# Kernel optimization log

Hardware: AMD Instinct MI355X
Metric: run time of the kernel (lower is better)

Reference implementation:

```python
import jax, jax.numpy as jnp
import numpy as np

T = 2048
C = 2048
N_HEAD = 16
HEAD_DIM = C // N_HEAD


def setup_inputs() -> dict:
    key = jax.random.key(0)
    k1, k2, k3 = jax.random.split(key, 3)
    x = jax.random.normal(k1, (T, C), dtype=jnp.float32)
    # eqx.nn.Linear weight convention: (out_features, in_features)
    W_attn = jax.random.normal(k2, (3 * C, C), dtype=jnp.float32) * (1.0 / np.sqrt(C))
    W_proj = jax.random.normal(k3, (C, C), dtype=jnp.float32) * (1.0 / np.sqrt(C))
    return {"x": x, "W_attn": W_attn, "W_proj": W_proj}


def reference(x, W_attn, W_proj):
    # qkv projection: (T, 3C)
    qkv = x @ W_attn.T
    q, k, v = jnp.split(qkv, 3, axis=-1)
    # reshape to (H, T, d)
    q = q.reshape(T, N_HEAD, HEAD_DIM).transpose(1, 0, 2)
    k = k.reshape(T, N_HEAD, HEAD_DIM).transpose(1, 0, 2)
    v = v.reshape(T, N_HEAD, HEAD_DIM).transpose(1, 0, 2)
    # scaled causal attention: (H, T, T)
    att = jnp.einsum('htd,hsd->hts', q, k)
    causal_mask = jnp.triu(jnp.ones((T, T), dtype=bool), k=1)  # mask future keys
    att = jnp.where(causal_mask, -jnp.inf, att)
    att = jax.nn.softmax(att / jnp.sqrt(jnp.float32(HEAD_DIM)), axis=-1)
    # attention output: (H, T, d) -> (T, C)
    out = jnp.einsum('hts,hsd->htd', att, v)
    out = out.transpose(1, 0, 2).reshape(T, C)
    return out @ W_proj.T
```

## Files before the change

### kernel.cpp

```cpp
#include <hip/hip_runtime.h>
#include <cstdint>

using bx8 = __attribute__((ext_vector_type(8))) __bf16;
using us8 = __attribute__((ext_vector_type(8))) unsigned short;
using fl8 = __attribute__((ext_vector_type(8))) float;
using fx4 = __attribute__((ext_vector_type(4))) float;

static __device__ inline unsigned short f2bf(float f) {
  unsigned u = __builtin_bit_cast(unsigned, f);
  unsigned r = 0x7FFFu + ((u >> 16) & 1u);
  return (unsigned short)((u + r) >> 16);
}
static __device__ inline float bf2f(unsigned short s) {
  return __builtin_bit_cast(float, (unsigned)s << 16);
}

static __device__ inline fx4 mfma16(bx8 a, bx8 b, fx4 c) {
  return __builtin_amdgcn_mfma_f32_16x16x32_bf16(a, b, c, 0, 0, 0);
}

static __device__ inline void gload16(const void* g, void* lds) {
  __builtin_amdgcn_global_load_lds(
      (const __attribute__((address_space(1))) void*)g,
      (__attribute__((address_space(3))) void*)lds,
      16, 0, 0);
}
#define VMCNT(n) asm volatile("s_waitcnt vmcnt(" #n ")" ::: "memory")
static __device__ inline void wave_barrier() {
  __builtin_amdgcn_sched_barrier(0);
  __builtin_amdgcn_s_barrier();
  __builtin_amdgcn_sched_barrier(0);
}

#define DPP_ROR(x, k) __builtin_bit_cast(float, __builtin_amdgcn_update_dpp( \
    __builtin_bit_cast(int, x), __builtin_bit_cast(int, x), 0x120 | (k), 0xF, 0xF, false))

static __device__ inline float rowmax16(float v) {
  v = fmaxf(v, DPP_ROR(v, 1));
  v = fmaxf(v, DPP_ROR(v, 2));
  v = fmaxf(v, DPP_ROR(v, 4));
  v = fmaxf(v, DPP_ROR(v, 8));
  return v;
}
static __device__ inline float rowsum16(float v) {
  v += DPP_ROR(v, 1);
  v += DPP_ROR(v, 2);
  v += DPP_ROR(v, 4);
  v += DPP_ROR(v, 8);
  return v;
}

__global__ __launch_bounds__(256) void f2b_kernel(const float* __restrict__ in,
                                                  unsigned short* __restrict__ out,
                                                  int n) {
  int i = (blockIdx.x * 256 + threadIdx.x) * 4;
  if (i >= n) return;
  float4 v = *reinterpret_cast<const float4*>(in + i);
  ushort4 o;
  o.x = f2bf(v.x); o.y = f2bf(v.y); o.z = f2bf(v.z); o.w = f2bf(v.w);
  *reinterpret_cast<ushort4*>(out + i) = o;
}

__global__ __launch_bounds__(512, 2) void gemm256(const unsigned short* __restrict__ A,
                                                  const unsigned short* __restrict__ B,
                                                  unsigned short* __restrict__ C,
                                                  int M, int N, int K) {
  __shared__ unsigned short lds[4][2][256 * 32];

  const int tid = threadIdx.x;
  const int w = tid >> 6, l = tid & 63;
  const int l16 = l & 15, lg = l >> 4;
  const int wr = w >> 2, wc = w & 3;
  const long mb = (long)blockIdx.y * 256, nb = (long)blockIdx.x * 256;

  const int lr = l >> 2;
  const int sw = (((l & 3) ^ (lr & 3)) * 8);
  const unsigned short* Ag = A + (mb + w * 32 + lr) * (long)K + sw;
  const unsigned short* Bg = B + (nb + w * 32 + lr) * (long)K + sw;

  const int rdcol = ((lg ^ (l16 & 3)) * 16);

  const fx4 fz = {0.f, 0.f, 0.f, 0.f};
  fx4 acc[8][4];
#pragma unroll
  for (int i = 0; i < 8; ++i)
#pragma unroll
    for (int j = 0; j < 4; ++j) acc[i][j] = fz;

  const int nt = K >> 5;

  auto stage = [&](int tp) {
    const int db = tp & 3;
    const unsigned short* as = Ag + tp * 32;
    const unsigned short* bs = Bg + tp * 32;
    char* al = (char*)&lds[db][0][0] + w * 32 * 64;
    char* bl = (char*)&lds[db][1][0] + w * 32 * 64;
    gload16(as, al);
    gload16(as + 16 * (long)K, al + 1024);
    gload16(bs, bl);
    gload16(bs + 16 * (long)K, bl + 1024);
  };

  auto compute = [&](int bt) {
    const char* Ab = (const char*)&lds[bt][0][0] + (wr * 128 + l16) * 64 + rdcol;
    const char* Bb = (const char*)&lds[bt][1][0] + (wc * 64 + l16) * 64 + rdcol;
    bx8 bf[4];
#pragma unroll
    for (int nf = 0; nf < 4; ++nf)
      bf[nf] = *reinterpret_cast<const bx8*>(Bb + nf * 1024);
    __builtin_amdgcn_s_setprio(1);
#pragma unroll
    for (int mf = 0; mf < 8; ++mf) {
      bx8 av = *reinterpret_cast<const bx8*>(Ab + mf * 1024);
#pragma unroll
      for (int nf = 0; nf < 4; ++nf)
        acc[mf][nf] = mfma16(av, bf[nf], acc[mf][nf]);
    }
    __builtin_amdgcn_s_setprio(0);
  };

  stage(0); stage(1); stage(2);
  VMCNT(8);
  wave_barrier();

  int t = 0;
  for (; t < nt - 3; ++t) {
    stage(t + 3);
    compute(t & 3);
    VMCNT(8);
    wave_barrier();
  }
  compute(t & 3); VMCNT(4); wave_barrier(); ++t;
  compute(t & 3); VMCNT(0); wave_barrier(); ++t;
  compute(t & 3);

#pragma unroll
  for (int mf = 0; mf < 8; ++mf)
#pragma unroll
    for (int nf = 0; nf < 4; ++nf)
#pragma unroll
      for (int r = 0; r < 4; ++r) {
        const long row = mb + wr * 128 + mf * 16 + lg * 4 + r;
        const long col = nb + wc * 64 + nf * 16 + l16;
        C[row * N + col] = f2bf(acc[mf][nf][r]);
      }
}

template <typename T> struct RegOf { using type = us8; };
template <> struct RegOf<float>  { using type = fl8; };

template <typename T>
static __device__ inline typename RegOf<T>::type load8(const T* p) {
  return *reinterpret_cast<const typename RegOf<T>::type*>(p);
}
static __device__ inline us8 toBf(us8 v) { return v; }
static __device__ inline us8 toBf(fl8 f) {
  us8 o;
#pragma unroll
  for (int j = 0; j < 8; ++j) {
    __bf16 b = (__bf16)f[j];
    o[j] = __builtin_bit_cast(unsigned short, b);
  }
  return o;
}

template <typename TA, typename TB, bool F32OUT>
__global__ __launch_bounds__(256) void gemm_bt(const TA* __restrict__ A,
                                               const TB* __restrict__ B,
                                               void* __restrict__ Cp,
                                               int M, int N, int K) {
  __shared__ alignas(16) unsigned short As[128 * 64];
  __shared__ alignas(16) unsigned short Bs[128 * 64];
  const int tid = threadIdx.x;
  const int w = tid >> 6, l = tid & 63;
  const int l16 = l & 15, lg = l >> 4;
  const int wr = w >> 1, wc = w & 1;
  const long mb = (long)blockIdx.y * 128, nb = (long)blockIdx.x * 128;

  const fx4 fz = {0.f, 0.f, 0.f, 0.f};
  fx4 acc[4][4];
#pragma unroll
  for (int i = 0; i < 4; ++i)
#pragma unroll
    for (int j = 0; j < 4; ++j) acc[i][j] = fz;

  const int sr  = tid >> 3;
  const int sc8 = (tid & 7) * 8;
  const int wbc = sc8 * 2;

  typename RegOf<TA>::type rA[4];
  typename RegOf<TB>::type rB[4];

#pragma unroll
  for (int p = 0; p < 4; ++p) {
    const int row = p * 32 + sr;
    rA[p] = load8(A + (mb + row) * (long)K + sc8);
    rB[p] = load8(B + (nb + row) * (long)K + sc8);
  }

  for (int k0 = 0; k0 < K; k0 += 64) {
    __syncthreads();
#pragma unroll
    for (int p = 0; p < 4; ++p) {
      const int row = p * 32 + sr;
      const int eo = row * 64 + ((wbc ^ ((row & 7) << 4)) >> 1);
      *reinterpret_cast<us8*>(&As[eo]) = toBf(rA[p]);
      *reinterpret_cast<us8*>(&Bs[eo]) = toBf(rB[p]);
    }
    if (k0 + 64 < K) {
#pragma unroll
      for (int p = 0; p < 4; ++p) {
        const int row = p * 32 + sr;
        rA[p] = load8(A + (mb + row) * (long)K + k0 + 64 + sc8);
        rB[p] = load8(B + (nb + row) * (long)K + k0 + 64 + sc8);
      }
    }
    __syncthreads();
#pragma unroll
    for (int kk = 0; kk < 2; ++kk) {
      bx8 a[4], b[4];
#pragma unroll
      for (int mf = 0; mf < 4; ++mf) {
        const int ra = wr * 64 + mf * 16 + l16;
        const int bc = kk * 64 + lg * 16;
        a[mf] = *reinterpret_cast<const bx8*>(&As[ra * 64 + ((bc ^ ((ra & 7) << 4)) >> 1)]);
      }
#pragma unroll
      for (int nf = 0; nf < 4; ++nf) {
        const int rb_ = wc * 64 + nf * 16 + l16;
        const int bc = kk * 64 + lg * 16;
        b[nf] = *reinterpret_cast<const bx8*>(&Bs[rb_ * 64 + ((bc ^ ((rb_ & 7) << 4)) >> 1)]);
      }
#pragma unroll
      for (int mf = 0; mf < 4; ++mf)
#pragma unroll
        for (int nf = 0; nf < 4; ++nf)
          acc[mf][nf] = mfma16(a[mf], b[nf], acc[mf][nf]);
    }
  }

#pragma unroll
  for (int mf = 0; mf < 4; ++mf)
#pragma unroll
    for (int nf = 0; nf < 4; ++nf)
#pragma unroll
      for (int r = 0; r < 4; ++r) {
        const long row = mb + wr * 64 + mf * 16 + lg * 4 + r;
        const long col = nb + wc * 64 + nf * 16 + l16;
        if (F32OUT)
          ((float*)Cp)[row * N + col] = acc[mf][nf][r];
        else
          ((unsigned short*)Cp)[row * N + col] = f2bf(acc[mf][nf][r]);
      }
}

__global__ __launch_bounds__(256) void fa_kernel(const unsigned short* __restrict__ qkv,
                                                 unsigned short* __restrict__ out,
                                                 unsigned short* __restrict__ Obuf,
                                                 float* __restrict__ ML) {
  __shared__ alignas(16) unsigned short Ks[64 * 136];
  __shared__ alignas(16) unsigned short Vt[128 * 72];
  __shared__ alignas(16) unsigned short Ps[4][16 * 72];

  const int id = blockIdx.x;
  int h, qt, t0, t1;
  bool partial;
  if (id < 512) {
    const int p = id >> 1, c = id & 1;
    qt = 31 - (p >> 4); h = p & 15;
    const int nt0 = (qt + 2) >> 1;
    t0 = c ? nt0 : 0;
    t1 = c ? (qt + 1) : nt0;
    partial = true;
  } else {
    const int s = id - 512;
    qt = 15 - (s >> 4); h = s & 15;
    t0 = 0; t1 = qt + 1;
    partial = false;
  }
  const int qb = qt * 64;

  const int tid = threadIdx.x;
  const int w = tid >> 6, l = tid & 63;
  const int l16 = l & 15, lg = l >> 4;
  const fx4 fz = {0.f, 0.f, 0.f, 0.f};

  const int kr = tid >> 4, kc8 = (tid & 15) * 8;
  const int kv = tid & 63, d0v = (tid >> 6) * 32;

  bx8 qf[4];
  {
    const long qrow = qb + w * 16 + l16;
    const unsigned short* qp = qkv + qrow * 6144L + h * 128 + lg * 8;
#pragma unroll
    for (int kc = 0; kc < 4; ++kc)
      qf[kc] = *reinterpret_cast<const bx8*>(qp + kc * 32);
  }

  fx4 o_acc[8];
#pragma unroll
  for (int i = 0; i < 8; ++i) o_acc[i] = fz;
  float m_r[4] = {-3e38f, -3e38f, -3e38f, -3e38f};
  float l_r[4] = {0.f, 0.f, 0.f, 0.f};

  us8 rK[4], rV[4];
  {
    const long kvb = (long)t0 * 64;
#pragma unroll
    for (int p = 0; p < 4; ++p)
      rK[p] = *reinterpret_cast<const us8*>(qkv + (kvb + p * 16 + kr) * 6144L + 2048 + h * 128 + kc8);
#pragma unroll
    for (int i = 0; i < 4; ++i)
      rV[i] = *reinterpret_cast<const us8*>(qkv + (kvb + kv) * 6144L + 4096 + h * 128 + d0v + i * 8);
  }

  for (int t = t0; t < t1; ++t) {
    __syncthreads();

#pragma unroll
    for (int p = 0; p < 4; ++p)
      *reinterpret_cast<us8*>(&Ks[(p * 16 + kr) * 136 + kc8]) = rK[p];
#pragma unroll
    for (int i = 0; i < 4; ++i)
#pragma unroll
      for (int j = 0; j < 8; ++j)
        Vt[(d0v + i * 8 + j) * 72 + kv] = rV[i][j];

    if (t + 1 < t1) {
      const long kvb = (long)(t + 1) * 64;
#pragma unroll
      for (int p = 0; p < 4; ++p)
        rK[p] = *reinterpret_cast<const us8*>(qkv + (kvb + p * 16 + kr) * 6144L + 2048 + h * 128 + kc8);
#pragma unroll
      for (int i = 0; i < 4; ++i)
        rV[i] = *reinterpret_cast<const us8*>(qkv + (kvb + kv) * 6144L + 4096 + h * 128 + d0v + i * 8);
    }
    __syncthreads();

    fx4 s[4];
#pragma unroll
    for (int nf = 0; nf < 4; ++nf) s[nf] = fz;
#pragma unroll
    for (int kc = 0; kc < 4; ++kc) {
#pragma unroll
      for (int nf = 0; nf < 4; ++nf) {
        const int rl = nf * 16 + l16;
        bx8 kb = *reinterpret_cast<const bx8*>(&Ks[rl * 136 + kc * 32 + lg * 8]);
        s[nf] = mfma16(qf[kc], kb, s[nf]);
      }
    }

    if (t == qt) {
#pragma unroll
      for (int nf = 0; nf < 4; ++nf) {
        const int kv_abs = t * 64 + nf * 16 + l16;
#pragma unroll
        for (int r = 0; r < 4; ++r) {
          const int q_abs = qb + w * 16 + lg * 4 + r;
          if (kv_abs > q_abs) s[nf][r] = -3e38f;
        }
      }
    }

    const float sc2 = 0.1275173831f;
    float pv[4][4];
#pragma unroll
    for (int r = 0; r < 4; ++r) {
      float rm = fmaxf(fmaxf(s[0][r], s[1][r]), fmaxf(s[2][r], s[3][r]));
      rm = rowmax16(rm);
      const float mn = fmaxf(m_r[r], rm);
      const float fac = exp2f((m_r[r] - mn) * sc2);
      m_r[r] = mn;
      float rs = 0.f;
#pragma unroll
      for (int nf = 0; nf < 4; ++nf) {
        const float p = exp2f((s[nf][r] - mn) * sc2);
        pv[nf][r] = p;
        rs += p;
      }
      rs = rowsum16(rs);
      l_r[r] = l_r[r] * fac + rs;
#pragma unroll
      for (int nf = 0; nf < 8; ++nf) o_acc[nf][r] *= fac;
    }

    unsigned short* psw = &Ps[w][0];
#pragma unroll
    for (int nf = 0; nf < 4; ++nf)
#pragma unroll
      for (int r = 0; r < 4; ++r)
        psw[(lg * 4 + r) * 72 + nf * 16 + l16] = f2bf(pv[nf][r]);

    bx8 pa[2];
#pragma unroll
    for (int kc = 0; kc < 2; ++kc)
      pa[kc] = *reinterpret_cast<const bx8*>(&psw[l16 * 72 + kc * 32 + lg * 8]);

#pragma unroll
    for (int nf = 0; nf < 8; ++nf) {
#pragma unroll
      for (int kc = 0; kc < 2; ++kc) {
        bx8 vb = *reinterpret_cast<const bx8*>(&Vt[(nf * 16 + l16) * 72 + kc * 32 + lg * 8]);
        o_acc[nf] = mfma16(pa[kc], vb, o_acc[nf]);
      }
    }
  }

  if (!partial) {
#pragma unroll
    for (int nf = 0; nf < 8; ++nf)
#pragma unroll
      for (int r = 0; r < 4; ++r) {
        const long row = qb + w * 16 + lg * 4 + r;
        const long col = h * 128 + nf * 16 + l16;
        out[row * 2048 + col] = f2bf(o_acc[nf][r] / l_r[r]);
      }
  } else {
    unsigned short* ob = Obuf + (long)id * 8192;
#pragma unroll
    for (int nf = 0; nf < 8; ++nf)
#pragma unroll
      for (int r = 0; r < 4; ++r) {
        const int row = w * 16 + lg * 4 + r;
        ob[row * 128 + nf * 16 + l16] = f2bf(o_acc[nf][r]);
      }
    if (l16 == 0) {
#pragma unroll
      for (int r = 0; r < 4; ++r) {
        const int row = w * 16 + lg * 4 + r;
        ML[((long)id * 64 + row) * 2 + 0] = m_r[r];
        ML[((long)id * 64 + row) * 2 + 1] = l_r[r];
      }
    }
  }
}

__global__ __launch_bounds__(256) void fa_combine(const unsigned short* __restrict__ Obuf,
                                                  const float* __restrict__ ML,
                                                  unsigned short* __restrict__ out) {
  const int p = blockIdx.x;
  const int qt = 31 - (p >> 4), h = p & 15;
  const int tid = threadIdx.x;
  const int row = tid >> 2;
  const int c0 = (tid & 3) * 32;

  const long idA = 2 * p, idB = 2 * p + 1;
  const float mA = ML[(idA * 64 + row) * 2 + 0];
  const float lA = ML[(idA * 64 + row) * 2 + 1];
  const float mB = ML[(idB * 64 + row) * 2 + 0];
  const float lB = ML[(idB * 64 + row) * 2 + 1];
  const float sc2 = 0.1275173831f;
  const float m = fmaxf(mA, mB);
  const float fA = exp2f((mA - m) * sc2);
  const float fB = exp2f((mB - m) * sc2);
  const float inv = 1.0f / (lA * fA + lB * fB);
  const float cA = fA * inv, cB = fB * inv;

  const unsigned short* oa = Obuf + idA * 8192 + row * 128 + c0;
  const unsigned short* obp = Obuf + idB * 8192 + row * 128 + c0;
  unsigned short* dst = out + (long)(qt * 64 + row) * 2048 + h * 128 + c0;
#pragma unroll
  for (int j = 0; j < 4; ++j) {
    us8 a = *reinterpret_cast<const us8*>(oa + j * 8);
    us8 b = *reinterpret_cast<const us8*>(obp + j * 8);
    ushort4 o0, o1;
    float v0, v1, v2, v3;
    v0 = bf2f(a[0]) * cA + bf2f(b[0]) * cB;
    v1 = bf2f(a[1]) * cA + bf2f(b[1]) * cB;
    v2 = bf2f(a[2]) * cA + bf2f(b[2]) * cB;
    v3 = bf2f(a[3]) * cA + bf2f(b[3]) * cB;
    o0 = {f2bf(v0), f2bf(v1), f2bf(v2), f2bf(v3)};
    v0 = bf2f(a[4]) * cA + bf2f(b[4]) * cB;
    v1 = bf2f(a[5]) * cA + bf2f(b[5]) * cB;
    v2 = bf2f(a[6]) * cA + bf2f(b[6]) * cB;
    v3 = bf2f(a[7]) * cA + bf2f(b[7]) * cB;
    o1 = {f2bf(v0), f2bf(v1), f2bf(v2), f2bf(v3)};
    *reinterpret_cast<ushort4*>(dst + j * 8) = o0;
    *reinterpret_cast<ushort4*>(dst + j * 8 + 4) = o1;
  }
}

extern "C" void kernel_launch(void* const* d_in, const int* in_sizes, int n_in,
                              void* d_out, int out_size, void* d_ws, size_t ws_size,
                              hipStream_t stream) {
  const float* x  = (const float*)d_in[0];
  const float* Wa = (const float*)d_in[1];
  const float* Wp = (const float*)d_in[2];
  float* out = (float*)d_out;
  char* ws = (char*)d_ws;

  unsigned short* wab   = (unsigned short*)(ws);
  unsigned short* qkvb  = (unsigned short*)(ws + (24ull << 20));
  unsigned short* xb    = (unsigned short*)(ws + (48ull << 20));
  unsigned short* Obuf  = (unsigned short*)(ws);
  float*          ML    = (float*)(ws + (8ull << 20));
  unsigned short* attnb = (unsigned short*)(ws + (48ull << 20));

  f2b_kernel<<<4096, 256, 0, stream>>>(x, xb, 2048 * 2048);
  f2b_kernel<<<12288, 256, 0, stream>>>(Wa, wab, 6144 * 2048);

  gemm256<<<dim3(24, 8), 512, 0, stream>>>(xb, wab, qkvb, 2048, 6144, 2048);

  fa_kernel<<<768, 256, 0, stream>>>(qkvb, attnb, Obuf, ML);

  fa_combine<<<256, 256, 0, stream>>>(Obuf, ML, attnb);

  gemm_bt<unsigned short, float, true><<<dim3(16, 16), 256, 0, stream>>>(attnb, Wp, (void*)out, 2048, 2048, 2048);
}
```

Before: 180.0 us.

## Split attention KV range into fixed 8-tile chunks with generalized combine

Every query tile's KV range is now split into chunks of at most 8 tiles, giving 1280 flash-attention blocks that all write partial outputs, with a combine kernel that merges up to four partials per tile. This balances the causal workload across more blocks. The change also adds a lazy rescale that skips the running-max update and accumulator rescaling when the new row max stays within a threshold. It also reorganises the V transpose into vectorised 4-element LDS stores and uses the native bf16 convert for P. The cost is extra partial-output traffic and a combine pass over all tiles, including ones with a single chunk.

Result: no change. 182.9 us (+1.6%).

```diff
diff --git a/kernel.cpp b/kernel.cpp
--- a/kernel.cpp
+++ b/kernel.cpp
@@ -3,6 +3,7 @@
 
 using bx8 = __attribute__((ext_vector_type(8))) __bf16;
 using us8 = __attribute__((ext_vector_type(8))) unsigned short;
+using us4 = __attribute__((ext_vector_type(4))) unsigned short;
 using fl8 = __attribute__((ext_vector_type(8))) float;
 using fx4 = __attribute__((ext_vector_type(4))) float;
 
@@ -255,7 +256,6 @@
 }
 
 __global__ __launch_bounds__(256) void fa_kernel(const unsigned short* __restrict__ qkv,
-                                                 unsigned short* __restrict__ out,
                                                  unsigned short* __restrict__ Obuf,
                                                  float* __restrict__ ML) {
   __shared__ alignas(16) unsigned short Ks[64 * 136];
@@ -263,21 +263,14 @@
   __shared__ alignas(16) unsigned short Ps[4][16 * 72];
 
   const int id = blockIdx.x;
-  int h, qt, t0, t1;
-  bool partial;
-  if (id < 512) {
-    const int p = id >> 1, c = id & 1;
-    qt = 31 - (p >> 4); h = p & 15;
-    const int nt0 = (qt + 2) >> 1;
-    t0 = c ? nt0 : 0;
-    t1 = c ? (qt + 1) : nt0;
-    partial = true;
-  } else {
-    const int s = id - 512;
-    qt = 15 - (s >> 4); h = s & 15;
-    t0 = 0; t1 = qt + 1;
-    partial = false;
-  }
+  const int h = id & 15, i = id >> 4;
+  int qt, ck;
+  if (i < 32)      { qt = 31 - (i >> 2); ck = i & 3; }
+  else if (i < 56) { const int j = i - 32; qt = 23 - j / 3; ck = j % 3; }
+  else if (i < 72) { const int j = i - 56; qt = 15 - (j >> 1); ck = j & 1; }
+  else             { qt = 7 - (i - 72); ck = 0; }
+  const int t0 = ck * 8;
+  const int t1 = min(t0 + 8, qt + 1);
   const int qb = qt * 64;
 
   const int tid = threadIdx.x;
@@ -286,7 +279,7 @@
   const fx4 fz = {0.f, 0.f, 0.f, 0.f};
 
   const int kr = tid >> 4, kc8 = (tid & 15) * 8;
-  const int kv = tid & 63, d0v = (tid >> 6) * 32;
+  const int kg = tid & 15, db = tid >> 4;
 
   bx8 qf[4];
   {
@@ -299,7 +292,7 @@
 
   fx4 o_acc[8];
 #pragma unroll
-  for (int i = 0; i < 8; ++i) o_acc[i] = fz;
+  for (int i2 = 0; i2 < 8; ++i2) o_acc[i2] = fz;
   float m_r[4] = {-3e38f, -3e38f, -3e38f, -3e38f};
   float l_r[4] = {0.f, 0.f, 0.f, 0.f};
 
@@ -310,9 +303,11 @@
     for (int p = 0; p < 4; ++p)
       rK[p] = *reinterpret_cast<const us8*>(qkv + (kvb + p * 16 + kr) * 6144L + 2048 + h * 128 + kc8);
 #pragma unroll
-    for (int i = 0; i < 4; ++i)
-      rV[i] = *reinterpret_cast<const us8*>(qkv + (kvb + kv) * 6144L + 4096 + h * 128 + d0v + i * 8);
-  }
+    for (int p = 0; p < 4; ++p)
+      rV[p] = *reinterpret_cast<const us8*>(qkv + (kvb + kg * 4 + p) * 6144L + 4096 + h * 128 + db * 8);
+  }
+
+  const float sc2 = 0.1275173831f;
 
   for (int t = t0; t < t1; ++t) {
     __syncthreads();
@@ -321,10 +316,10 @@
     for (int p = 0; p < 4; ++p)
       *reinterpret_cast<us8*>(&Ks[(p * 16 + kr) * 136 + kc8]) = rK[p];
 #pragma unroll
-    for (int i = 0; i < 4; ++i)
-#pragma unroll
-      for (int j = 0; j < 8; ++j)
-        Vt[(d0v + i * 8 + j) * 72 + kv] = rV[i][j];
+    for (int j = 0; j < 8; ++j) {
+      us4 vw = {rV[0][j], rV[1][j], rV[2][j], rV[3][j]};
+      *reinterpret_cast<us4*>(&Vt[(db * 8 + j) * 72 + kg * 4]) = vw;
+    }
 
     if (t + 1 < t1) {
       const long kvb = (long)(t + 1) * 64;
@@ -332,8 +327,8 @@
       for (int p = 0; p < 4; ++p)
         rK[p] = *reinterpret_cast<const us8*>(qkv + (kvb + p * 16 + kr) * 6144L + 2048 + h * 128 + kc8);
 #pragma unroll
-      for (int i = 0; i < 4; ++i)
-        rV[i] = *reinterpret_cast<const us8*>(qkv + (kvb + kv) * 6144L + 4096 + h * 128 + d0v + i * 8);
+      for (int p = 0; p < 4; ++p)
+        rV[p] = *reinterpret_cast<const us8*>(qkv + (kvb + kg * 4 + p) * 6144L + 4096 + h * 128 + db * 8);
     }
     __syncthreads();
 
@@ -362,26 +357,44 @@
       }
     }
 
-    const float sc2 = 0.1275173831f;
-    float pv[4][4];
+    float rm_[4];
+    bool st = true;
 #pragma unroll
     for (int r = 0; r < 4; ++r) {
       float rm = fmaxf(fmaxf(s[0][r], s[1][r]), fmaxf(s[2][r], s[3][r]));
-      rm = rowmax16(rm);
-      const float mn = fmaxf(m_r[r], rm);
-      const float fac = exp2f((m_r[r] - mn) * sc2);
-      m_r[r] = mn;
-      float rs = 0.f;
-#pragma unroll
-      for (int nf = 0; nf < 4; ++nf) {
-        const float p = exp2f((s[nf][r] - mn) * sc2);
-        pv[nf][r] = p;
-        rs += p;
-      }
-      rs = rowsum16(rs);
-      l_r[r] = l_r[r] * fac + rs;
-#pragma unroll
-      for (int nf = 0; nf < 8; ++nf) o_acc[nf][r] *= fac;
+      rm_[r] = rowmax16(rm);
+      st = st && (rm_[r] - m_r[r] <= 62.7f);
+    }
+    float pv[4][4];
+    if (__all(st ? 1 : 0)) {
+#pragma unroll
+      for (int r = 0; r < 4; ++r) {
+        float rs = 0.f;
+#pragma unroll
+        for (int nf = 0; nf < 4; ++nf) {
+          const float p = exp2f((s[nf][r] - m_r[r]) * sc2);
+          pv[nf][r] = p;
+          rs += p;
+        }
+        l_r[r] += rowsum16(rs);
+      }
+    } else {
+#pragma unroll
+      for (int r = 0; r < 4; ++r) {
+        const float mn = fmaxf(m_r[r], rm_[r]);
+        const float fac = exp2f((m_r[r] - mn) * sc2);
+        m_r[r] = mn;
+        float rs = 0.f;
+#pragma unroll
+        for (int nf = 0; nf < 4; ++nf) {
+          const float p = exp2f((s[nf][r] - mn) * sc2);
+          pv[nf][r] = p;
+          rs += p;
+        }
+        l_r[r] = l_r[r] * fac + rowsum16(rs);
+#pragma unroll
+        for (int nf = 0; nf < 8; ++nf) o_acc[nf][r] *= fac;
+      }
     }
 
     unsigned short* psw = &Ps[w][0];
@@ -389,7 +402,8 @@
     for (int nf = 0; nf < 4; ++nf)
 #pragma unroll
       for (int r = 0; r < 4; ++r)
-        psw[(lg * 4 + r) * 72 + nf * 16 + l16] = f2bf(pv[nf][r]);
+        psw[(lg * 4 + r) * 72 + nf * 16 + l16] =
+            __builtin_bit_cast(unsigned short, (__bf16)pv[nf][r]);
 
     bx8 pa[2];
 #pragma unroll
@@ -406,31 +420,20 @@
     }
   }
 
-  if (!partial) {
-#pragma unroll
-    for (int nf = 0; nf < 8; ++nf)
-#pragma unroll
-      for (int r = 0; r < 4; ++r) {
-        const long row = qb + w * 16 + lg * 4 + r;
-        const long col = h * 128 + nf * 16 + l16;
-        out[row * 2048 + col] = f2bf(o_acc[nf][r] / l_r[r]);
-      }
-  } else {
-    unsigned short* ob = Obuf + (long)id * 8192;
-#pragma unroll
-    for (int nf = 0; nf < 8; ++nf)
-#pragma unroll
-      for (int r = 0; r < 4; ++r) {
-        const int row = w * 16 + lg * 4 + r;
-        ob[row * 128 + nf * 16 + l16] = f2bf(o_acc[nf][r]);
-      }
-    if (l16 == 0) {
-#pragma unroll
-      for (int r = 0; r < 4; ++r) {
-        const int row = w * 16 + lg * 4 + r;
-        ML[((long)id * 64 + row) * 2 + 0] = m_r[r];
-        ML[((long)id * 64 + row) * 2 + 1] = l_r[r];
-      }
+  unsigned short* ob = Obuf + (long)id * 8192;
+#pragma unroll
+  for (int nf = 0; nf < 8; ++nf)
+#pragma unroll
+    for (int r = 0; r < 4; ++r) {
+      const int row = w * 16 + lg * 4 + r;
+      ob[row * 128 + nf * 16 + l16] = f2bf(o_acc[nf][r]);
+    }
+  if (l16 == 0) {
+#pragma unroll
+    for (int r = 0; r < 4; ++r) {
+      const int row = w * 16 + lg * 4 + r;
+      ML[((long)id * 64 + row) * 2 + 0] = m_r[r];
+      ML[((long)id * 64 + row) * 2 + 1] = l_r[r];
     }
   }
 }
@@ -439,44 +442,72 @@
                                                   const float* __restrict__ ML,
                                                   unsigned short* __restrict__ out) {
   const int p = blockIdx.x;
-  const int qt = 31 - (p >> 4), h = p & 15;
+  const int qt = p >> 4, h = p & 15;
+  const int nc = (qt + 8) >> 3;
   const int tid = threadIdx.x;
   const int row = tid >> 2;
   const int c0 = (tid & 3) * 32;
-
-  const long idA = 2 * p, idB = 2 * p + 1;
-  const float mA = ML[(idA * 64 + row) * 2 + 0];
-  const float lA = ML[(idA * 64 + row) * 2 + 1];
-  const float mB = ML[(idB * 64 + row) * 2 + 0];
-  const float lB = ML[(idB * 64 + row) * 2 + 1];
   const float sc2 = 0.1275173831f;
-  const float m = fmaxf(mA, mB);
-  const float fA = exp2f((mA - m) * sc2);
-  const float fB = exp2f((mB - m) * sc2);
-  const float inv = 1.0f / (lA * fA + lB * fB);
-  const float cA = fA * inv, cB = fB * inv;
-
-  const unsigned short* oa = Obuf + idA * 8192 + row * 128 + c0;
-  const unsigned short* obp = Obuf + idB * 8192 + row * 128 + c0;
+
+  int ids[4];
+#pragma unroll
+  for (int k = 0; k < 4; ++k) {
+    int ib;
+    if (qt >= 24)      ib = (31 - qt) * 4 + k;
+    else if (qt >= 16) ib = 32 + (23 - qt) * 3 + k;
+    else if (qt >= 8)  ib = 56 + (15 - qt) * 2 + k;
+    else               ib = 72 + (7 - qt);
+    ids[k] = ib * 16 + h;
+  }
+
+  float mk[4], lk[4];
+  float m = -3e38f;
+#pragma unroll
+  for (int k = 0; k < 4; ++k)
+    if (k < nc) {
+      mk[k] = ML[((long)ids[k] * 64 + row) * 2 + 0];
+      lk[k] = ML[((long)ids[k] * 64 + row) * 2 + 1];
+      m = fmaxf(m, mk[k]);
+    }
+  float fk[4], denom = 0.f;
+#pragma unroll
+  for (int k = 0; k < 4; ++k)
+    if (k < nc) {
+      fk[k] = exp2f((mk[k] - m) * sc2);
+      denom += lk[k] * fk[k];
+    }
+  const float inv = 1.0f / denom;
+
+  float acc[32];
+#pragma unroll
+  for (int j = 0; j < 32; ++j) acc[j] = 0.f;
+#pragma unroll
+  for (int k = 0; k < 4; ++k)
+    if (k < nc) {
+      const unsigned short* ob = Obuf + (long)ids[k] * 8192 + row * 128 + c0;
+      const float f = fk[k];
+#pragma unroll
+      for (int jj = 0; jj < 4; ++jj) {
+        us8 a = *reinterpret_cast<const us8*>(ob + jj * 8);
+#pragma unroll
+        for (int j2 = 0; j2 < 8; ++j2) acc[jj * 8 + j2] += bf2f(a[j2]) * f;
+      }
+    }
+
   unsigned short* dst = out + (long)(qt * 64 + row) * 2048 + h * 128 + c0;
 #pragma unroll
-  for (int j = 0; j < 4; ++j) {
-    us8 a = *reinterpret_cast<const us8*>(oa + j * 8);
-    us8 b = *reinterpret_cast<const us8*>(obp + j * 8);
+  for (int jj = 0; jj < 4; ++jj) {
     ushort4 o0, o1;
-    float v0, v1, v2, v3;
-    v0 = bf2f(a[0]) * cA + bf2f(b[0]) * cB;
-    v1 = bf2f(a[1]) * cA + bf2f(b[1]) * cB;
-    v2 = bf2f(a[2]) * cA + bf2f(b[2]) * cB;
-    v3 = bf2f(a[3]) * cA + bf2f(b[3]) * cB;
-    o0 = {f2bf(v0), f2bf(v1), f2bf(v2), f2bf(v3)};
-    v0 = bf2f(a[4]) * cA + bf2f(b[4]) * cB;
-    v1 = bf2f(a[5]) * cA + bf2f(b[5]) * cB;
-    v2 = bf2f(a[6]) * cA + bf2f(b[6]) * cB;
-    v3 = bf2f(a[7]) * cA + bf2f(b[7]) * cB;
-    o1 = {f2bf(v0), f2bf(v1), f2bf(v2), f2bf(v3)};
-    *reinterpret_cast<ushort4*>(dst + j * 8) = o0;
-    *reinterpret_cast<ushort4*>(dst + j * 8 + 4) = o1;
+    o0.x = f2bf(acc[jj * 8 + 0] * inv);
+    o0.y = f2bf(acc[jj * 8 + 1] * inv);
+    o0.z = f2bf(acc[jj * 8 + 2] * inv);
+    o0.w = f2bf(acc[jj * 8 + 3] * inv);
+    o1.x = f2bf(acc[jj * 8 + 4] * inv);
+    o1.y = f2bf(acc[jj * 8 + 5] * inv);
+    o1.z = f2bf(acc[jj * 8 + 6] * inv);
+    o1.w = f2bf(acc[jj * 8 + 7] * inv);
+    *reinterpret_cast<ushort4*>(dst + jj * 8) = o0;
+    *reinterpret_cast<ushort4*>(dst + jj * 8 + 4) = o1;
   }
 }
 
@@ -493,7 +524,7 @@
   unsigned short* qkvb  = (unsigned short*)(ws + (24ull << 20));
   unsigned short* xb    = (unsigned short*)(ws + (48ull << 20));
   unsigned short* Obuf  = (unsigned short*)(ws);
-  float*          ML    = (float*)(ws + (8ull << 20));
+  float*          ML    = (float*)(ws + (20ull << 20));
   unsigned short* attnb = (unsigned short*)(ws + (48ull << 20));
 
   f2b_kernel<<<4096, 256, 0, stream>>>(x, xb, 2048 * 2048);
@@ -501,9 +532,9 @@
 
   gemm256<<<dim3(24, 8), 512, 0, stream>>>(xb, wab, qkvb, 2048, 6144, 2048);
 
-  fa_kernel<<<768, 256, 0, stream>>>(qkvb, attnb, Obuf, ML);
-
-  fa_combine<<<256, 256, 0, stream>>>(Obuf, ML, attnb);
+  fa_kernel<<<1280, 256, 0, stream>>>(qkvb, Obuf, ML);
+
+  fa_combine<<<512, 256, 0, stream>>>(Obuf, ML, attnb);
 
   gemm_bt<unsigned short, float, true><<<dim3(16, 16), 256, 0, stream>>>(attnb, Wp, (void*)out, 2048, 2048, 2048);
 }
```
